# Performance work log

Measured on AMD Instinct MI355X. Metric: run time of the kernel, lower is better.

The kernel has to match this reference:

```python
import jax, jax.numpy as jnp
import numpy as np

SCALES = (5, 15, 40)


def _hamilton(a, b):
    # a, b: (..., 4) quaternions in [w, x, y, z]
    aw, ax, ay, az = a[..., 0], a[..., 1], a[..., 2], a[..., 3]
    bw, bx, by, bz = b[..., 0], b[..., 1], b[..., 2], b[..., 3]
    return jnp.stack([
        aw * bw - ax * bx - ay * by - az * bz,
        aw * bx + ax * bw + ay * bz - az * by,
        aw * by - ax * bz + ay * bw + az * bx,
        aw * bz + ax * by - ay * bx + az * bw,
    ], axis=-1)


def _bearing_quaternions(xyz):
    # xyz: (B, F, P, 3) -> bearing quaternions (B, F, P, 4)
    bbox_min = xyz.min(axis=2)
    bbox_max = xyz.max(axis=2)
    centroids = (bbox_min + bbox_max) * 0.5  # (B, F, 3)
    d = xyz - centroids[:, :, None, :]
    d = d / jnp.clip(jnp.linalg.norm(d, axis=-1, keepdims=True), 1e-12)
    dot = jnp.clip(d[..., 1], -1.0 + 1e-7, 1.0 - 1e-7)
    half = jnp.arccos(dot) * 0.5
    axis = jnp.stack([d[..., 2], jnp.zeros_like(d[..., 0]), -d[..., 0]], axis=-1)
    axis = axis / jnp.clip(jnp.linalg.norm(axis, axis=-1, keepdims=True), 1e-12)
    s = jnp.sin(half)
    return jnp.stack([jnp.cos(half), axis[..., 0] * s, axis[..., 1] * s, axis[..., 2] * s], axis=-1)


def _torch_lower_median(x):
    flat = jnp.sort(x.reshape(-1))
    return flat[(flat.shape[0] - 1) // 2]


def _bearing_qcc_multiscale(points_4d, num_frames):
    B, F, P, _ = points_4d.shape
    xyz = points_4d[..., :3]  # (B, F, P, 3)
    bq = _bearing_quaternions(xyz)  # (B, F, P, 4)

    # Per-transition relative quaternion q_fwd = q_tgt * conj(q_src), vectorized over T = F-1
    conj_sign = jnp.array([1.0, -1.0, -1.0, -1.0], dtype=points_4d.dtype)
    q_src = bq[:, :-1] * conj_sign  # conj, (B, T, P, 4)
    q_tgt = bq[:, 1:]
    q_fwd = _hamilton(q_tgt, q_src)
    q_fwd = q_fwd / jnp.clip(jnp.linalg.norm(q_fwd, axis=-1, keepdims=True), 1e-12)

    # KNN on source-frame xyz for all transitions at once (topk is sorted desc,
    # so smaller-k neighborhoods are prefixes of the max-k result)
    pts = xyz[:, :-1]  # (B, T, P, 3)
    sq = jnp.sum(pts * pts, axis=-1)  # (B, T, P)
    neg_dist = 2.0 * jnp.einsum('btpc,btqc->btpq', pts, pts) - sq[..., :, None] - sq[..., None, :]
    kmax = max(SCALES)
    _, idx = jax.lax.top_k(neg_dist, kmax)  # (B, T, P, kmax)

    # Gather neighbor quaternions: (B, T, P, kmax, 4)
    b_ix = jnp.arange(B)[:, None, None, None]
    t_ix = jnp.arange(F - 1)[None, :, None, None]
    nbr_q = q_fwd[b_ix, t_ix, idx]

    dots = jnp.abs(jnp.sum(q_fwd[..., None, :] * nbr_q, axis=-1))
    dots = jnp.clip(dots, 0.0, 1.0 - 1e-7)
    geo = 2.0 * jnp.arccos(dots)  # (B, T, P, kmax)

    rigidities = []
    for k in SCALES:
        mean_inc = geo[..., :k].mean(axis=-1).mean(axis=1)  # (B, P)
        scale = jnp.clip(_torch_lower_median(mean_inc), 1e-6)
        rig = jnp.where(mean_inc.max() > 0,
                        jnp.exp(-mean_inc / scale),
                        jnp.ones_like(mean_inc))  # (B, P)
        rig = jnp.broadcast_to(rig[:, None, :], (B, F, P)).reshape(B, 1, F * P)
        rigidities.append(rig)
    return jnp.concatenate(rigidities, axis=1)  # (B, len(SCALES), F*P)


def setup_inputs() -> dict:
    key = jax.random.key(0)
    B, F, P = 2, 8, 2048
    points_4d = jax.random.normal(key, (B, F, P, 4), dtype=jnp.float32)
    return {"points_4d": points_4d, "num_frames": F}


def reference(points_4d, num_frames):
    return _bearing_qcc_multiscale(points_4d, num_frames)
```

## Files before the change

kernel.cpp:

```cpp
#include <hip/hip_runtime.h>
#include <math.h>

typedef unsigned long long u64;
typedef unsigned int u32;

#define B_ 2
#define F_ 8
#define P_ 2048
#define T_ 7
#define ROWS (B_*T_*P_)
#define SENT_OU 0xFFFFFFFFu

#define CED(arr,a,b) do { double _x=arr[a], _y=arr[b]; arr[a]=fmin(_x,_y); arr[b]=fmax(_x,_y); } while(0)

__device__ __forceinline__ void sort8d(double* k) {
  CED(k,0,1); CED(k,2,3); CED(k,4,5); CED(k,6,7);
  CED(k,0,2); CED(k,1,3); CED(k,4,6); CED(k,5,7);
  CED(k,1,2); CED(k,5,6);
  CED(k,0,4); CED(k,1,5); CED(k,2,6); CED(k,3,7);
  CED(k,2,4); CED(k,3,5);
  CED(k,1,2); CED(k,3,4); CED(k,5,6);
}

__device__ __forceinline__ void low8(double* A, const double* Bv) {
#pragma unroll
  for (int i = 0; i < 8; ++i) A[i] = fmin(A[i], Bv[7-i]);
#pragma unroll
  for (int st = 4; st >= 1; st >>= 1) {
#pragma unroll
    for (int i = 0; i < 8; ++i) {
      if ((i & st) == 0) { CED(A, i, i + st); }
    }
  }
}

__device__ __forceinline__ u32 bfly16_min_u32(u32 x) {
  u32 t;
  t = (u32)__builtin_amdgcn_update_dpp((int)x,(int)x,0x0B1,0xF,0xF,false); x = t<x?t:x;
  t = (u32)__builtin_amdgcn_update_dpp((int)x,(int)x,0x04E,0xF,0xF,false); x = t<x?t:x;
  t = (u32)__builtin_amdgcn_update_dpp((int)x,(int)x,0x141,0xF,0xF,false); x = t<x?t:x;
  t = (u32)__builtin_amdgcn_update_dpp((int)x,(int)x,0x140,0xF,0xF,false); x = t<x?t:x;
  return x;
}
__device__ __forceinline__ float bfly16_sum_f32(float x) {
  float t;
  t = __uint_as_float((u32)__builtin_amdgcn_update_dpp((int)__float_as_uint(x),(int)__float_as_uint(x),0x0B1,0xF,0xF,false)); x += t;
  t = __uint_as_float((u32)__builtin_amdgcn_update_dpp((int)__float_as_uint(x),(int)__float_as_uint(x),0x04E,0xF,0xF,false)); x += t;
  t = __uint_as_float((u32)__builtin_amdgcn_update_dpp((int)__float_as_uint(x),(int)__float_as_uint(x),0x141,0xF,0xF,false)); x += t;
  t = __uint_as_float((u32)__builtin_amdgcn_update_dpp((int)__float_as_uint(x),(int)__float_as_uint(x),0x140,0xF,0xF,false)); x += t;
  return x;
}

__global__ __launch_bounds__(256) void kA_bearing(const float4* __restrict__ pts,
                                                  float4* __restrict__ bq,
                                                  float4* __restrict__ pts2) {
  int bf = blockIdx.x;
  const float4* base = pts + (size_t)bf * P_;
  int tid = threadIdx.x;
  float x[8], y[8], z[8];
  float mnx =  INFINITY, mny =  INFINITY, mnz =  INFINITY;
  float mxx = -INFINITY, mxy = -INFINITY, mxz = -INFINITY;
#pragma unroll
  for (int i = 0; i < 8; ++i) {
    float4 v = base[tid + i*256];
    x[i]=v.x; y[i]=v.y; z[i]=v.z;
    mnx=fminf(mnx,v.x); mny=fminf(mny,v.y); mnz=fminf(mnz,v.z);
    mxx=fmaxf(mxx,v.x); mxy=fmaxf(mxy,v.y); mxz=fmaxf(mxz,v.z);
  }
#pragma unroll
  for (int off = 32; off >= 1; off >>= 1) {
    mnx=fminf(mnx,__shfl_xor(mnx,off)); mny=fminf(mny,__shfl_xor(mny,off)); mnz=fminf(mnz,__shfl_xor(mnz,off));
    mxx=fmaxf(mxx,__shfl_xor(mxx,off)); mxy=fmaxf(mxy,__shfl_xor(mxy,off)); mxz=fmaxf(mxz,__shfl_xor(mxz,off));
  }
  __shared__ float red[4][6];
  int wid = tid >> 6, lane = tid & 63;
  if (lane == 0) { red[wid][0]=mnx; red[wid][1]=mny; red[wid][2]=mnz;
                   red[wid][3]=mxx; red[wid][4]=mxy; red[wid][5]=mxz; }
  __syncthreads();
  mnx=fminf(fminf(red[0][0],red[1][0]),fminf(red[2][0],red[3][0]));
  mny=fminf(fminf(red[0][1],red[1][1]),fminf(red[2][1],red[3][1]));
  mnz=fminf(fminf(red[0][2],red[1][2]),fminf(red[2][2],red[3][2]));
  mxx=fmaxf(fmaxf(red[0][3],red[1][3]),fmaxf(red[2][3],red[3][3]));
  mxy=fmaxf(fmaxf(red[0][4],red[1][4]),fmaxf(red[2][4],red[3][4]));
  mxz=fmaxf(fmaxf(red[0][5],red[1][5]),fmaxf(red[2][5],red[3][5]));
  float cx=(mnx+mxx)*0.5f, cy=(mny+mxy)*0.5f, cz=(mnz+mxz)*0.5f;
#pragma unroll
  for (int i = 0; i < 8; ++i) {
    float dx=x[i]-cx, dy=y[i]-cy, dz=z[i]-cz;
    float n = sqrtf(((dx*dx) + dy*dy) + dz*dz);
    n = fmaxf(n, 1e-12f);
    float dxn = dx/n, dyn = dy/n, dzn = dz/n;
    float dotc = fminf(fmaxf(dyn, -0.99999990f), 0.99999990f);
    float half = acosf(dotc) * 0.5f;
    float an = sqrtf(dzn*dzn + dxn*dxn);
    an = fmaxf(an, 1e-12f);
    float axx = dzn/an, axz = (-dxn)/an;
    float s = sinf(half), w = cosf(half);
    bq[(size_t)bf*P_ + tid + i*256] = make_float4(w, axx*s, 0.f, axz*s);
    float qs = fmaf(x[i],x[i], fmaf(y[i],y[i], z[i]*z[i]));
    pts2[(size_t)bf*P_ + tid + i*256] = make_float4(x[i], y[i], z[i], qs);
  }
}

__global__ __launch_bounds__(256) void kB_qfwd(const float4* __restrict__ bq,
                                               float4* __restrict__ qf) {
  int i = blockIdx.x*256 + threadIdx.x;
  int p = i & (P_-1);
  int t = (i >> 11) % T_;
  int b = i / (T_*P_);
  float4 s = bq[((size_t)(b*F_ + t))*P_ + p];
  float4 a = bq[((size_t)(b*F_ + t + 1))*P_ + p];
  float aw=a.x, ax=a.y, ay=a.z, az=a.w;
  float bw=s.x, bx=-s.y, by=-s.z, bz=-s.w;
  float w  = ((aw*bw - ax*bx) - ay*by) - az*bz;
  float xo = ((aw*bx + ax*bw) + ay*bz) - az*by;
  float yo = ((aw*by - ax*bz) + ay*bw) + az*bx;
  float zo = ((aw*bz + ax*by) - ay*bx) + az*bw;
  float n = sqrtf(((w*w + xo*xo) + yo*yo) + zo*zo);
  n = fmaxf(n, 1e-12f);
  qf[i] = make_float4(w/n, xo/n, yo/n, zo/n);
}

__device__ __forceinline__ double mkkey(float4 c, u32 q,
                                        float px, float py, float pz, float ps) {
  float dot = fmaf(px, c.x, fmaf(py, c.y, pz*c.z));
  float v = (2.f*dot - ps) - c.w;
  float nd = -v;
  u32 u = __float_as_uint(nd);
  u32 ou = (u & 0x80000000u) ? ~u : (u | 0x80000000u);
  return __longlong_as_double((long long)(0x4000000000000000ull | ((u64)ou << 16) | q));
}

__device__ __forceinline__ void popstep(u32 (&OU)[8], u32 (&IX)[8],
                                        u32& LOU, u32& LIX, u32& CAP, int imod,
                                        int slot, const float4* __restrict__ pbase,
                                        float px, float py, float pz, float ps) {
  if (__any(OU[0] == SENT_OU)) {
    bool need = (OU[0] == SENT_OU);
    u64 lastK = ((u64)LOU << 16) | LIX;
    u64 best = ~0ull;
    for (int j = 0; j < 128; ++j) {
      u32 q = (u32)(j*16 + slot);
      float4 c = pbase[q];
      float dot = fmaf(px, c.x, fmaf(py, c.y, pz*c.z));
      float v = (2.f*dot - ps) - c.w;
      u32 u = __float_as_uint(-v);
      u32 ou = (u & 0x80000000u) ? ~u : (u | 0x80000000u);
      u64 kk = ((u64)ou << 16) | q;
      if (kk > lastK && kk < best) best = kk;
    }
    if (need && best != ~0ull) { OU[0] = (u32)(best >> 16); IX[0] = (u32)(best & 0xffffu); }
  }
  u32 qmin = bfly16_min_u32(OU[0]);
  bool meq = (OU[0] == qmin);
  u32 tt   = meq ? IX[0] : 0xFFFFFFFFu;
  u32 widx = bfly16_min_u32(tt);
  bool iam = meq && (IX[0] == widx);
  CAP = (slot == imod) ? widx : CAP;
  LOU = iam ? qmin : LOU;
  LIX = iam ? widx : LIX;
#pragma unroll
  for (int jj = 0; jj < 7; ++jj) {
    OU[jj] = iam ? OU[jj+1] : OU[jj];
    IX[jj] = iam ? IX[jj+1] : IX[jj];
  }
  OU[7] = iam ? SENT_OU : OU[7];
}

__global__ __launch_bounds__(256) void kC_select(const float4* __restrict__ pts2,
                                                 const float4* __restrict__ qf,
                                                 float* __restrict__ S) {
  int lane = threadIdx.x & 63;
  int wid  = threadIdx.x >> 6;
  int slot = lane & 15;
  int quarter = lane >> 4;
  int gid = blockIdx.x * 16 + wid * 4;
  int p0 = gid & (P_-1);
  int bt = gid >> 11;
  int t  = bt % T_;
  int b  = bt / T_;
  const float4* pbase = pts2 + (size_t)(b*F_ + t) * P_;

  int prow = p0 + quarter;
  float4 pw = pbase[prow];
  float px=pw.x, py=pw.y, pz=pw.z, ps=pw.w;

  double acc[8];
#pragma unroll
  for (int j = 0; j < 8; ++j) acc[j] = __builtin_huge_val();
#pragma unroll 2
  for (int batch = 0; batch < 16; ++batch) {
    int qb = batch*128 + slot;
    float4 c[8];
#pragma unroll
    for (int u = 0; u < 8; ++u) c[u] = pbase[qb + u*16];
    double k[8];
#pragma unroll
    for (int u = 0; u < 8; ++u) k[u] = mkkey(c[u], (u32)(qb + u*16), px,py,pz,ps);
    sort8d(k);
    low8(acc, k);
  }

  u32 OU[8], IX[8];
#pragma unroll
  for (int j = 0; j < 8; ++j) {
    u64 bb = (u64)__double_as_longlong(acc[j]);
    OU[j] = (u32)(bb >> 16); IX[j] = (u32)(bb & 0xffffu);
  }

  u32 lou=0, lix=0, cap1=0, cap2=0, cap3=0;

#pragma unroll 1
  for (int i = 0; i < 16; ++i)
    popstep(OU, IX, lou, lix, cap1, i, slot, pbase, px,py,pz,ps);
#pragma unroll 1
  for (int i = 0; i < 16; ++i)
    popstep(OU, IX, lou, lix, cap2, i, slot, pbase, px,py,pz,ps);
#pragma unroll 1
  for (int i = 0; i < 8; ++i)
    popstep(OU, IX, lou, lix, cap3, i, slot, pbase, px,py,pz,ps);

  int row = bt*P_ + prow;
  const float4* qbt = qf + (size_t)bt * P_;
  float4 qp = qf[row];

  float4 n; float d;
  n = qbt[cap1]; d = ((qp.x*n.x + qp.y*n.y) + qp.z*n.z) + qp.w*n.w;
  float g1 = 2.f * acosf(fminf(fabsf(d), 0.99999990f));
  n = qbt[cap2]; d = ((qp.x*n.x + qp.y*n.y) + qp.z*n.z) + qp.w*n.w;
  float g2 = 2.f * acosf(fminf(fabsf(d), 0.99999990f));
  n = qbt[cap3]; d = ((qp.x*n.x + qp.y*n.y) + qp.z*n.z) + qp.w*n.w;
  float g3 = (slot < 8) ? 2.f * acosf(fminf(fabsf(d), 0.99999990f)) : 0.f;

  float s40 = bfly16_sum_f32(g1 + g2 + g3);
  float s15 = bfly16_sum_f32((slot < 15) ? g1 : 0.f);
  float s5  = bfly16_sum_f32((slot < 5)  ? g1 : 0.f);

  if (slot == 0) {
    S[0*ROWS + row] = s5  / 5.f;
    S[1*ROWS + row] = s15 / 15.f;
    S[2*ROWS + row] = s40 / 40.f;
  }
}

__global__ __launch_bounds__(1024) void kE_final(const float* __restrict__ S,
                                                 float* __restrict__ out) {
  int k = blockIdx.x;
  int tid = threadIdx.x;
  __shared__ float srt[4096];
  const float* Sk = S + (size_t)k * ROWS;
  float m[4];
#pragma unroll
  for (int u = 0; u < 4; ++u) {
    int j = tid + u*1024;
    int b = j >> 11, p = j & 2047;
    float acc = 0.f;
#pragma unroll
    for (int t = 0; t < 7; ++t) acc += Sk[(b*7 + t)*2048 + p];
    m[u] = acc / 7.f;
    srt[j] = m[u];
  }
  __syncthreads();
  for (int size = 2; size <= 4096; size <<= 1) {
    for (int stride = size >> 1; stride > 0; stride >>= 1) {
      for (int c = tid; c < 2048; c += 1024) {
        int i = 2*c - (c & (stride - 1));
        int j = i + stride;
        bool up = ((i & size) == 0);
        float a = srt[i], bb = srt[j];
        if ((a > bb) == up) { srt[i] = bb; srt[j] = a; }
      }
      __syncthreads();
    }
  }
  float scale = fmaxf(srt[2047], 1e-6f);
  bool pos = srt[4095] > 0.f;
#pragma unroll
  for (int u = 0; u < 4; ++u) {
    int j = tid + u*1024;
    int b = j >> 11, p = j & 2047;
    float r = pos ? expf(-m[u]/scale) : 1.f;
    float* ob = out + ((size_t)(b*3 + k)*8)*2048 + p;
#pragma unroll
    for (int f = 0; f < 8; ++f) ob[f*2048] = r;
  }
}

extern "C" void kernel_launch(void* const* d_in, const int* in_sizes, int n_in,
                              void* d_out, int out_size, void* d_ws, size_t ws_size,
                              hipStream_t stream) {
  (void)in_sizes; (void)n_in; (void)out_size; (void)ws_size;
  const float4* pts = (const float4*)d_in[0];
  float* ws = (float*)d_ws;
  float4* bq   = (float4*)ws;
  float4* qfw  = (float4*)(ws + 131072);
  float*  S    = ws + 131072 + 114688;
  float4* pts2 = (float4*)(ws + 131072 + 114688 + 86016);
  float*  out = (float*)d_out;

  hipLaunchKernelGGL(kA_bearing, dim3(B_*F_), dim3(256), 0, stream, pts, bq, pts2);
  hipLaunchKernelGGL(kB_qfwd,    dim3(ROWS/256), dim3(256), 0, stream, bq, qfw);
  hipLaunchKernelGGL(kC_select,  dim3(ROWS/16), dim3(256), 0, stream, pts2, qfw, S);
  hipLaunchKernelGGL(kE_final,   dim3(3), dim3(1024), 0, stream, S, out);
}
```

Baseline: 142.6 us.

## Use integer u64 sort keys, speculative fast pop with exact fallback, single-block final

Replaces the double-as-integer min/max sorting networks with native u64 compare-exchange and seeds the accumulator from the first batch. The per-pop refill scan is replaced by a speculative merge that only falls back to the exact refill path when a lane has exhausted its 8 local candidates. The final median/sort kernel now processes all three scales in one block instead of three. The single-block final stage gives up cross-block parallelism, and u64 compares may cost more than double fmin/fmax on this hardware.

```diff
diff --git a/kernel.cpp b/kernel.cpp
--- a/kernel.cpp
+++ b/kernel.cpp
@@ -11,25 +11,25 @@
 #define ROWS (B_*T_*P_)
 #define SENT_OU 0xFFFFFFFFu
 
-#define CED(arr,a,b) do { double _x=arr[a], _y=arr[b]; arr[a]=fmin(_x,_y); arr[b]=fmax(_x,_y); } while(0)
-
-__device__ __forceinline__ void sort8d(double* k) {
-  CED(k,0,1); CED(k,2,3); CED(k,4,5); CED(k,6,7);
-  CED(k,0,2); CED(k,1,3); CED(k,4,6); CED(k,5,7);
-  CED(k,1,2); CED(k,5,6);
-  CED(k,0,4); CED(k,1,5); CED(k,2,6); CED(k,3,7);
-  CED(k,2,4); CED(k,3,5);
-  CED(k,1,2); CED(k,3,4); CED(k,5,6);
-}
-
-__device__ __forceinline__ void low8(double* A, const double* Bv) {
-#pragma unroll
-  for (int i = 0; i < 8; ++i) A[i] = fmin(A[i], Bv[7-i]);
+#define CEU(arr,a,b) do { u64 _x=arr[a], _y=arr[b]; bool _s=(_y<_x); arr[a]=_s?_y:_x; arr[b]=_s?_x:_y; } while(0)
+
+__device__ __forceinline__ void sort8u(u64* k) {
+  CEU(k,0,1); CEU(k,2,3); CEU(k,4,5); CEU(k,6,7);
+  CEU(k,0,2); CEU(k,1,3); CEU(k,4,6); CEU(k,5,7);
+  CEU(k,1,2); CEU(k,5,6);
+  CEU(k,0,4); CEU(k,1,5); CEU(k,2,6); CEU(k,3,7);
+  CEU(k,2,4); CEU(k,3,5);
+  CEU(k,1,2); CEU(k,3,4); CEU(k,5,6);
+}
+
+__device__ __forceinline__ void low8u(u64* A, const u64* Bv) {
+#pragma unroll
+  for (int i = 0; i < 8; ++i) { u64 b = Bv[7-i]; A[i] = (b < A[i]) ? b : A[i]; }
 #pragma unroll
   for (int st = 4; st >= 1; st >>= 1) {
 #pragma unroll
     for (int i = 0; i < 8; ++i) {
-      if ((i & st) == 0) { CED(A, i, i + st); }
+      if ((i & st) == 0) { CEU(A, i, i + st); }
     }
   }
 }
@@ -121,20 +121,20 @@
   qf[i] = make_float4(w/n, xo/n, yo/n, zo/n);
 }
 
-__device__ __forceinline__ double mkkey(float4 c, u32 q,
-                                        float px, float py, float pz, float ps) {
+__device__ __forceinline__ u64 mkkey(float4 c, u32 q,
+                                     float px, float py, float pz, float ps) {
   float dot = fmaf(px, c.x, fmaf(py, c.y, pz*c.z));
   float v = (2.f*dot - ps) - c.w;
   float nd = -v;
   u32 u = __float_as_uint(nd);
   u32 ou = (u & 0x80000000u) ? ~u : (u | 0x80000000u);
-  return __longlong_as_double((long long)(0x4000000000000000ull | ((u64)ou << 16) | q));
-}
-
-__device__ __forceinline__ void popstep(u32 (&OU)[8], u32 (&IX)[8],
-                                        u32& LOU, u32& LIX, u32& CAP, int imod,
-                                        int slot, const float4* __restrict__ pbase,
-                                        float px, float py, float pz, float ps) {
+  return ((u64)ou << 16) | q;
+}
+
+__device__ __forceinline__ void popstep_exact(u32 (&OU)[8], u32 (&IX)[8],
+                                              u32& LOU, u32& LIX, u32& CAP, int imod,
+                                              int slot, const float4* __restrict__ pbase,
+                                              float px, float py, float pz, float ps) {
   if (__any(OU[0] == SENT_OU)) {
     bool need = (OU[0] == SENT_OU);
     u64 lastK = ((u64)LOU << 16) | LIX;
@@ -142,11 +142,7 @@
     for (int j = 0; j < 128; ++j) {
       u32 q = (u32)(j*16 + slot);
       float4 c = pbase[q];
-      float dot = fmaf(px, c.x, fmaf(py, c.y, pz*c.z));
-      float v = (2.f*dot - ps) - c.w;
-      u32 u = __float_as_uint(-v);
-      u32 ou = (u & 0x80000000u) ? ~u : (u | 0x80000000u);
-      u64 kk = ((u64)ou << 16) | q;
+      u64 kk = mkkey(c, q, px,py,pz,ps);
       if (kk > lastK && kk < best) best = kk;
     }
     if (need && best != ~0ull) { OU[0] = (u32)(best >> 16); IX[0] = (u32)(best & 0xffffu); }
@@ -159,6 +155,23 @@
   CAP = (slot == imod) ? widx : CAP;
   LOU = iam ? qmin : LOU;
   LIX = iam ? widx : LIX;
+#pragma unroll
+  for (int jj = 0; jj < 7; ++jj) {
+    OU[jj] = iam ? OU[jj+1] : OU[jj];
+    IX[jj] = iam ? IX[jj+1] : IX[jj];
+  }
+  OU[7] = iam ? SENT_OU : OU[7];
+}
+
+__device__ __forceinline__ void popstep_fast(u32 (&OU)[8], u32 (&IX)[8],
+                                             u32& CAP, u32& popped, int imod, int slot) {
+  u32 qmin = bfly16_min_u32(OU[0]);
+  bool meq = (OU[0] == qmin);
+  u32 tt   = meq ? IX[0] : 0xFFFFFFFFu;
+  u32 widx = bfly16_min_u32(tt);
+  bool iam = meq && (IX[0] == widx);
+  CAP = (slot == imod) ? widx : CAP;
+  popped += iam ? 1u : 0u;
 #pragma unroll
   for (int jj = 0; jj < 7; ++jj) {
     OU[jj] = iam ? OU[jj+1] : OU[jj];
@@ -185,40 +198,63 @@
   float4 pw = pbase[prow];
   float px=pw.x, py=pw.y, pz=pw.z, ps=pw.w;
 
-  double acc[8];
-#pragma unroll
-  for (int j = 0; j < 8; ++j) acc[j] = __builtin_huge_val();
+  u64 acc[8];
+  {
+    u64 k0[8];
+#pragma unroll
+    for (int u = 0; u < 8; ++u) { float4 c = pbase[u*16 + slot];
+      k0[u] = mkkey(c, (u32)(u*16 + slot), px,py,pz,ps); }
+    sort8u(k0);
+#pragma unroll
+    for (int j = 0; j < 8; ++j) acc[j] = k0[j];
+  }
 #pragma unroll 2
-  for (int batch = 0; batch < 16; ++batch) {
+  for (int batch = 1; batch < 16; ++batch) {
     int qb = batch*128 + slot;
     float4 c[8];
 #pragma unroll
     for (int u = 0; u < 8; ++u) c[u] = pbase[qb + u*16];
-    double k[8];
+    u64 k[8];
 #pragma unroll
     for (int u = 0; u < 8; ++u) k[u] = mkkey(c[u], (u32)(qb + u*16), px,py,pz,ps);
-    sort8d(k);
-    low8(acc, k);
-  }
-
-  u32 OU[8], IX[8];
+    sort8u(k);
+    low8u(acc, k);
+  }
+
+  u32 OU[8], IX[8], BOU[8], BIX[8];
 #pragma unroll
   for (int j = 0; j < 8; ++j) {
-    u64 bb = (u64)__double_as_longlong(acc[j]);
-    OU[j] = (u32)(bb >> 16); IX[j] = (u32)(bb & 0xffffu);
-  }
-
-  u32 lou=0, lix=0, cap1=0, cap2=0, cap3=0;
+    OU[j] = (u32)(acc[j] >> 16); IX[j] = (u32)(acc[j] & 0xffffu);
+    BOU[j] = OU[j]; BIX[j] = IX[j];
+  }
+
+  u32 cap1=0, cap2=0, cap3=0, popped=0;
 
 #pragma unroll 1
   for (int i = 0; i < 16; ++i)
-    popstep(OU, IX, lou, lix, cap1, i, slot, pbase, px,py,pz,ps);
+    popstep_fast(OU, IX, cap1, popped, i, slot);
 #pragma unroll 1
   for (int i = 0; i < 16; ++i)
-    popstep(OU, IX, lou, lix, cap2, i, slot, pbase, px,py,pz,ps);
+    popstep_fast(OU, IX, cap2, popped, i, slot);
 #pragma unroll 1
   for (int i = 0; i < 8; ++i)
-    popstep(OU, IX, lou, lix, cap3, i, slot, pbase, px,py,pz,ps);
+    popstep_fast(OU, IX, cap3, popped, i, slot);
+
+  if (__any(popped >= 8u)) {
+#pragma unroll
+    for (int j = 0; j < 8; ++j) { OU[j] = BOU[j]; IX[j] = BIX[j]; }
+    u32 lou = 0, lix = 0;
+    cap1 = cap2 = cap3 = 0;
+#pragma unroll 1
+    for (int i = 0; i < 16; ++i)
+      popstep_exact(OU, IX, lou, lix, cap1, i, slot, pbase, px,py,pz,ps);
+#pragma unroll 1
+    for (int i = 0; i < 16; ++i)
+      popstep_exact(OU, IX, lou, lix, cap2, i, slot, pbase, px,py,pz,ps);
+#pragma unroll 1
+    for (int i = 0; i < 8; ++i)
+      popstep_exact(OU, IX, lou, lix, cap3, i, slot, pbase, px,py,pz,ps);
+  }
 
   int row = bt*P_ + prow;
   const float4* qbt = qf + (size_t)bt * P_;
@@ -245,20 +281,22 @@
 
 __global__ __launch_bounds__(1024) void kE_final(const float* __restrict__ S,
                                                  float* __restrict__ out) {
-  int k = blockIdx.x;
   int tid = threadIdx.x;
-  __shared__ float srt[4096];
-  const float* Sk = S + (size_t)k * ROWS;
-  float m[4];
-#pragma unroll
-  for (int u = 0; u < 4; ++u) {
-    int j = tid + u*1024;
-    int b = j >> 11, p = j & 2047;
-    float acc = 0.f;
-#pragma unroll
-    for (int t = 0; t < 7; ++t) acc += Sk[(b*7 + t)*2048 + p];
-    m[u] = acc / 7.f;
-    srt[j] = m[u];
+  __shared__ float srt[3][4096];
+  float m[3][4];
+#pragma unroll
+  for (int k = 0; k < 3; ++k) {
+    const float* Sk = S + (size_t)k * ROWS;
+#pragma unroll
+    for (int u = 0; u < 4; ++u) {
+      int j = tid + u*1024;
+      int b = j >> 11, p = j & 2047;
+      float acc = 0.f;
+#pragma unroll
+      for (int t = 0; t < 7; ++t) acc += Sk[(b*7 + t)*2048 + p];
+      m[k][u] = acc / 7.f;
+      srt[k][j] = m[k][u];
+    }
   }
   __syncthreads();
   for (int size = 2; size <= 4096; size <<= 1) {
@@ -267,22 +305,28 @@
         int i = 2*c - (c & (stride - 1));
         int j = i + stride;
         bool up = ((i & size) == 0);
-        float a = srt[i], bb = srt[j];
-        if ((a > bb) == up) { srt[i] = bb; srt[j] = a; }
+#pragma unroll
+        for (int k = 0; k < 3; ++k) {
+          float a = srt[k][i], bb = srt[k][j];
+          if ((a > bb) == up) { srt[k][i] = bb; srt[k][j] = a; }
+        }
       }
       __syncthreads();
     }
   }
-  float scale = fmaxf(srt[2047], 1e-6f);
-  bool pos = srt[4095] > 0.f;
-#pragma unroll
-  for (int u = 0; u < 4; ++u) {
-    int j = tid + u*1024;
-    int b = j >> 11, p = j & 2047;
-    float r = pos ? expf(-m[u]/scale) : 1.f;
-    float* ob = out + ((size_t)(b*3 + k)*8)*2048 + p;
-#pragma unroll
-    for (int f = 0; f < 8; ++f) ob[f*2048] = r;
+#pragma unroll
+  for (int k = 0; k < 3; ++k) {
+    float scale = fmaxf(srt[k][2047], 1e-6f);
+    bool pos = srt[k][4095] > 0.f;
+#pragma unroll
+    for (int u = 0; u < 4; ++u) {
+      int j = tid + u*1024;
+      int b = j >> 11, p = j & 2047;
+      float r = pos ? expf(-m[k][u]/scale) : 1.f;
+      float* ob = out + ((size_t)(b*3 + k)*8)*2048 + p;
+#pragma unroll
+      for (int f = 0; f < 8; ++f) ob[f*2048] = r;
+    }
   }
 }
 
@@ -301,5 +345,5 @@
   hipLaunchKernelGGL(kA_bearing, dim3(B_*F_), dim3(256), 0, stream, pts, bq, pts2);
   hipLaunchKernelGGL(kB_qfwd,    dim3(ROWS/256), dim3(256), 0, stream, bq, qfw);
   hipLaunchKernelGGL(kC_select,  dim3(ROWS/16), dim3(256), 0, stream, pts2, qfw, S);
-  hipLaunchKernelGGL(kE_final,   dim3(3), dim3(1024), 0, stream, S, out);
-}
+  hipLaunchKernelGGL(kE_final,   dim3(1), dim3(1024), 0, stream, S, out);
+}
```

Result: slower. 211.8 us (+48.6%).
